# Kernel tuning notes

Hardware: AMD Instinct MI355X
Metric: run time of the kernel (lower is better)

The kernel has to match this reference:

```python
import jax, jax.numpy as jnp
import numpy as np

NUM_NODES = 80000
V_GLOBALS = 50000
N = 32      # grapharea_size
D = 300     # feature dim
R = 4       # num relations
E = 64      # edges per timestep
B, T = 2, 64


def setup_inputs() -> dict:
    key = jax.random.key(0)
    ks = jax.random.split(key, 10)
    return {
        "x_indices": jax.random.randint(ks[0], (B, T, N), 0, NUM_NODES, dtype=jnp.int32),
        "edge_index": jax.random.randint(ks[1], (B, T, 2, E), 0, N, dtype=jnp.int32),
        "edge_type": jax.random.randint(ks[2], (B, T, E), 0, R, dtype=jnp.int32),
        "X": jax.random.normal(ks[3], (NUM_NODES, D), jnp.float32) * 0.1,
        "conv_W": jax.random.normal(ks[4], (R, D, D), jnp.float32) * (1.0 / np.sqrt(D)),
        "W_0": jax.random.normal(ks[5], (D, D), jnp.float32) * (1.0 / np.sqrt(D)),
        "update_gate_W": jax.random.normal(ks[6], (N * D, D), jnp.float32) * (1.0 / np.sqrt(N * D)),
        "update_gate_U": jax.random.normal(ks[7], (D, D), jnp.float32) * (1.0 / np.sqrt(D)),
        "lin_w": jax.random.normal(ks[8], (V_GLOBALS, D), jnp.float32) * (1.0 / np.sqrt(D)),
        "lin_b": jax.random.normal(ks[9], (V_GLOBALS,), jnp.float32) * 0.01,
    }


def _rgcn_step(X, conv_W, W_0, Wg, Ug, lin_w, lin_b, mem, idx, ei, et):
    # gather grapharea features: [N, D]
    gx = X[idx]
    src, dst = ei[0], ei[1]
    n = gx.shape[0]
    r = conv_W.shape[0]
    # per-relation linear transform: [R, N, D]
    xw = jnp.einsum('nd,rde->rne', gx, conv_W)
    # edge-type masks emulate split_edge_index: [R, E]
    mask = (et[None, :] == jnp.arange(r, dtype=et.dtype)[:, None]).astype(gx.dtype)
    # GCN symmetric normalization with self-loops (deg includes self-loop weight 1)
    deg = jax.vmap(lambda w: jax.ops.segment_sum(w, dst, num_segments=n))(mask) + 1.0  # [R, N]
    dis = jax.lax.rsqrt(deg)
    norm = dis[:, src] * dis[:, dst] * mask                      # [R, E]
    msgs = xw[:, src, :] * norm[..., None]                       # [R, E, D]
    agg = jax.vmap(lambda m: jax.ops.segment_sum(m, dst, num_segments=n))(msgs)
    agg = agg + xw * (dis ** 2)[..., None]                       # self-loop messages
    composite = agg.sum(0)                                       # sum over relations, [N, D]
    # eye(N) @ (gx @ W_0) == gx @ W_0
    proposed = composite + gx @ W_0
    # GRU-style update gate from flattened grapharea + previous memory's first node
    u = jax.nn.sigmoid(gx.reshape(-1) @ Wg + mem[0] @ Ug)        # [D]
    new = u[None, :] * proposed + (1.0 - u[None, :]) * mem       # [N, D]
    x1 = jax.nn.leaky_relu(new)[0]                               # current node, [D]
    logits = x1 @ lin_w.T + lin_b                                # [V]
    return new, jax.nn.log_softmax(logits)


def reference(x_indices, edge_index, edge_type, X, conv_W, W_0, update_gate_W, update_gate_U, lin_w, lin_b):
    b, t, n = x_indices.shape
    s = b * t
    idxs = x_indices.reshape(s, n)
    eis = edge_index.reshape(s, 2, -1)
    ets = edge_type.reshape(s, -1)

    def step(mem, inp):
        idx, ei, et = inp
        new, logp = _rgcn_step(X, conv_W, W_0, update_gate_W, update_gate_U,
                               lin_w, lin_b, mem, idx, ei, et)
        # memory carry is a non-grad buffer updated via .data.copy_ in torch
        return jax.lax.stop_gradient(new), logp

    mem0 = jnp.zeros((n, X.shape[1]), X.dtype)
    _, preds_globals = jax.lax.scan(step, mem0, (idxs, eis, ets))  # [S, V]
    preds_senses = jnp.zeros((s,), X.dtype)  # include_senses=False -> stacked zeros
    return preds_globals, preds_senses
```

## Files before the change

kernel.cpp:

```cpp
#include <hip/hip_runtime.h>

#define S 128
#define N 32
#define D 300
#define DP 320
#define E 64
#define R 4
#define V 50000
#define VP 50048
#define ND 9600
#define KY 1504
#define DPAD 304

typedef unsigned short ushortT;
typedef __attribute__((ext_vector_type(8))) short short8;
typedef __attribute__((ext_vector_type(4))) short short4v;
typedef __attribute__((ext_vector_type(4))) float floatx4;
typedef __attribute__((ext_vector_type(19))) float floatx19;

__device__ inline float bf2f(ushortT h) {
    unsigned u = ((unsigned)h) << 16;
    float f;
    __builtin_memcpy(&f, &u, 4);
    return f;
}

__device__ inline float bfbits_lo(unsigned u) {
    unsigned b = u << 16;
    float f;
    __builtin_memcpy(&f, &b, 4);
    return f;
}

__device__ inline float bfbits_hi(unsigned u) {
    unsigned b = u & 0xffff0000u;
    float f;
    __builtin_memcpy(&f, &b, 4);
    return f;
}

__device__ inline ushortT f2bf(float f) {
    unsigned u;
    __builtin_memcpy(&u, &f, 4);
    unsigned r = (u + 0x7fffu + ((u >> 16) & 1u)) >> 16;
    return (ushortT)r;
}

__device__ inline float ldf(const void* p, size_t i, int isb) {
    return isb ? bf2f(((const ushortT*)p)[i]) : ((const float*)p)[i];
}

__device__ inline float rdlane(float v, int lane) {
    int iv;
    __builtin_memcpy(&iv, &v, 4);
    int r = __builtin_amdgcn_readlane(iv, lane);
    float f;
    __builtin_memcpy(&f, &r, 4);
    return f;
}

__global__ void k_detect(const void* X, int* flag) {
    __shared__ int bad;
    if (threadIdx.x == 0) bad = 0;
    __syncthreads();
    const ushortT* p = (const ushortT*)X;
    int b = 0;
    for (int i = threadIdx.x; i < 4096; i += 256) {
        float v = bf2f(p[i]);
        if (!(v > -2.f && v < 2.f)) b = 1;
    }
    if (b) atomicOr(&bad, 1);
    __syncthreads();
    if (threadIdx.x == 0) flag[0] = bad ? 0 : 1;
}

__global__ void k_gatherb(const int* __restrict__ flag, const int* __restrict__ xi,
                          const void* __restrict__ X, ushortT* __restrict__ gxb) {
    int isb = flag[0];
    int sn = blockIdx.x;
    int d = threadIdx.x;
    if (d < D) {
        int node = xi[sn];
        ushortT v = isb ? ((const ushortT*)X)[(size_t)node * D + d]
                        : f2bf(((const float*)X)[(size_t)node * D + d]);
        gxb[(size_t)sn * D + d] = v;
    }
}

__global__ void k_twg(const int* __restrict__ flag, const void* __restrict__ Wg,
                      ushortT* __restrict__ wgt) {
    int isb = flag[0];
    __shared__ float tile[32][33];
    int k0 = blockIdx.x * 32, d0 = blockIdx.y * 32;
    int tx = threadIdx.x & 31, ty = threadIdx.x >> 5;
    for (int i = ty; i < 32; i += 8) {
        int d = d0 + tx;
        tile[i][tx] = (d < D) ? ldf(Wg, (size_t)(k0 + i) * D + d, isb) : 0.f;
    }
    __syncthreads();
    for (int i = ty; i < 32; i += 8) {
        int d = d0 + i;
        if (d < DPAD) wgt[(size_t)d * ND + k0 + tx] = f2bf(tile[tx][i]);
    }
}

__global__ void k_tws(const int* __restrict__ flag, const void* __restrict__ convW,
                      const void* __restrict__ W0, ushortT* __restrict__ wst) {
    int isb = flag[0];
    __shared__ float tile[32][33];
    int k0 = blockIdx.x * 32, d0 = blockIdx.y * 32;
    int tx = threadIdx.x & 31, ty = threadIdx.x >> 5;
    for (int i = ty; i < 32; i += 8) {
        int kp = k0 + i, d = d0 + tx;
        float v = 0.f;
        if (d < D && kp < 1500)
            v = (kp < 1200) ? ldf(convW, (size_t)kp * D + d, isb)
                            : ldf(W0, (size_t)(kp - 1200) * D + d, isb);
        tile[i][tx] = v;
    }
    __syncthreads();
    for (int i = ty; i < 32; i += 8) {
        int d = d0 + i;
        if (d < DPAD) wst[(size_t)d * KY + k0 + tx] = f2bf(tile[tx][i]);
    }
}

__global__ void k_yb(const ushortT* __restrict__ gxb, const int* __restrict__ ei,
                     const int* __restrict__ et, ushortT* __restrict__ yb) {
    int s = blockIdx.x;
    int t = threadIdx.x;
    __shared__ int se[E], de[E], te[E];
    __shared__ float disv[R][N];
    if (t < E) {
        se[t] = ei[(size_t)s * 2 * E + t];
        de[t] = ei[(size_t)s * 2 * E + E + t];
        te[t] = et[(size_t)s * E + t];
    }
    __syncthreads();
    if (t < R * N) {
        int r = t >> 5, n = t & 31;
        float c = 1.f;
        for (int e = 0; e < E; ++e) c += (te[e] == r && de[e] == n) ? 1.f : 0.f;
        disv[r][n] = rsqrtf(c);
    }
    __syncthreads();
    if (t < D) {
        const ushortT* g = gxb + (size_t)s * ND;
        float g0 = bf2f(g[t]);
        float yy[R];
#pragma unroll
        for (int r = 0; r < R; ++r) yy[r] = g0 * disv[r][0] * disv[r][0];
        for (int e = 0; e < E; ++e) {
            if (de[e] == 0) {
                int r = te[e];
                yy[r] += disv[r][se[e]] * disv[r][0] * bf2f(g[(size_t)se[e] * D + t]);
            }
        }
#pragma unroll
        for (int r = 0; r < R; ++r) yb[(size_t)s * KY + r * D + t] = f2bf(yy[r]);
        yb[(size_t)s * KY + 4 * D + t] = g[t];
    }
    if (t < 4) yb[(size_t)s * KY + 1500 + t] = 0;
}

__global__ __launch_bounds__(256) void k_gemm(const ushortT* __restrict__ A, int lda,
                                              const ushortT* __restrict__ Bt, int ldb,
                                              float* __restrict__ C, int ldc, int ncols,
                                              int kchunks, int per) {
    int wave = threadIdx.x >> 6, lane = threadIdx.x & 63;
    int col = lane & 15, quad = lane >> 4;
    int m0 = blockIdx.x * 16, n0 = blockIdx.y * 16;
    int z = blockIdx.z;
    int kbeg = z * per;
    int kend = kbeg + per;
    if (kend > kchunks) kend = kchunks;
    floatx4 acc = {0.f, 0.f, 0.f, 0.f};
    const ushortT* ap = A + (size_t)(m0 + col) * lda + quad * 8;
    const ushortT* bp = Bt + (size_t)(n0 + col) * ldb + quad * 8;
    for (int kc = kbeg + wave; kc < kend; kc += 4) {
        short8 a = *(const short8*)(ap + kc * 32);
        short8 b = *(const short8*)(bp + kc * 32);
        acc = __builtin_amdgcn_mfma_f32_16x16x32_bf16(a, b, acc, 0, 0, 0);
    }
    __shared__ float red[4][64][4];
#pragma unroll
    for (int i = 0; i < 4; ++i) red[wave][lane][i] = acc[i];
    __syncthreads();
    if (wave == 0) {
#pragma unroll
        for (int i = 0; i < 4; ++i) {
            float v = red[0][lane][i] + red[1][lane][i] + red[2][lane][i] + red[3][lane][i];
            int m = m0 + quad * 4 + i;
            int n = n0 + col;
            if (n < ncols) C[(size_t)z * S * ldc + (size_t)m * ldc + n] = v;
        }
    }
}

__global__ void k_red(const float* __restrict__ part, float* __restrict__ out, int n, int nz) {
    int i = blockIdx.x * 256 + threadIdx.x;
    if (i < n) {
        float v = 0.f;
        for (int z = 0; z < nz; ++z) v += part[(size_t)z * n + i];
        out[i] = v;
    }
}

__global__ __attribute__((amdgpu_flat_work_group_size(512, 512), amdgpu_waves_per_eu(2, 2))) void
k_scan(const int* __restrict__ flag, const float* __restrict__ a, const float* __restrict__ P0,
       const void* __restrict__ Ug, ushortT* __restrict__ x1p) {
    int isb = flag[0];
    int t = threadIdx.x;
    int w = t >> 6, lane = t & 63;
    int kbase = w * 38;
    int myk = kbase + lane;
    bool red_ok = (lane < 38) && (myk < D);
    int d4 = 256 + lane;
    bool d4ok = d4 < D;
    floatx19 A0, A1, A2, A3, A4, B0, B1, B2, B3, B4;
    if (isb) {
        const ushortT* U = (const ushortT*)Ug;
#pragma unroll
        for (int j = 0; j < 19; ++j) {
            int k1 = kbase + j, k2 = k1 + 19;
            bool k2ok = k2 < D;
            A0[j] = bf2f(U[k1 * D + lane]);
            A1[j] = bf2f(U[k1 * D + 64 + lane]);
            A2[j] = bf2f(U[k1 * D + 128 + lane]);
            A3[j] = bf2f(U[k1 * D + 192 + lane]);
            A4[j] = d4ok ? bf2f(U[k1 * D + d4]) : 0.f;
            B0[j] = k2ok ? bf2f(U[k2 * D + lane]) : 0.f;
            B1[j] = k2ok ? bf2f(U[k2 * D + 64 + lane]) : 0.f;
            B2[j] = k2ok ? bf2f(U[k2 * D + 128 + lane]) : 0.f;
            B3[j] = k2ok ? bf2f(U[k2 * D + 192 + lane]) : 0.f;
            B4[j] = (k2ok && d4ok) ? bf2f(U[k2 * D + d4]) : 0.f;
        }
    } else {
        const float* U = (const float*)Ug;
#pragma unroll
        for (int j = 0; j < 19; ++j) {
            int k1 = kbase + j, k2 = k1 + 19;
            bool k2ok = k2 < D;
            A0[j] = U[k1 * D + lane];
            A1[j] = U[k1 * D + 64 + lane];
            A2[j] = U[k1 * D + 128 + lane];
            A3[j] = U[k1 * D + 192 + lane];
            A4[j] = d4ok ? U[k1 * D + d4] : 0.f;
            B0[j] = k2ok ? U[k2 * D + lane] : 0.f;
            B1[j] = k2ok ? U[k2 * D + 64 + lane] : 0.f;
            B2[j] = k2ok ? U[k2 * D + 128 + lane] : 0.f;
            B3[j] = k2ok ? U[k2 * D + 192 + lane] : 0.f;
            B4[j] = (k2ok && d4ok) ? U[k2 * D + d4] : 0.f;
        }
    }
    for (int i = t; i < S * 20; i += 512) {
        int s = i / 20, d = 300 + (i % 20);
        x1p[(size_t)s * DP + d] = 0;
    }
    __shared__ float part[2][8][320];
    float mreg = 0.f;
    int buf = 0;
    for (int s = 0; s < S; ++s) {
        float av = 0.f, pv = 0.f;
        if (red_ok) {
            av = a[s * D + myk];
            pv = P0[s * D + myk];
        }
        float acc0 = 0.f, acc1 = 0.f, acc2 = 0.f, acc3 = 0.f, acc4 = 0.f;
#pragma unroll
        for (int j = 0; j < 19; ++j) {
            float sm = rdlane(mreg, j);
            acc0 = fmaf(sm, A0[j], acc0);
            acc1 = fmaf(sm, A1[j], acc1);
            acc2 = fmaf(sm, A2[j], acc2);
            acc3 = fmaf(sm, A3[j], acc3);
            acc4 = fmaf(sm, A4[j], acc4);
        }
#pragma unroll
        for (int j = 0; j < 19; ++j) {
            float sm = rdlane(mreg, 19 + j);
            acc0 = fmaf(sm, B0[j], acc0);
            acc1 = fmaf(sm, B1[j], acc1);
            acc2 = fmaf(sm, B2[j], acc2);
            acc3 = fmaf(sm, B3[j], acc3);
            acc4 = fmaf(sm, B4[j], acc4);
        }
        part[buf][w][lane] = acc0;
        part[buf][w][64 + lane] = acc1;
        part[buf][w][128 + lane] = acc2;
        part[buf][w][192 + lane] = acc3;
        part[buf][w][256 + lane] = acc4;
        __syncthreads();
        if (red_ok) {
            float pr = av;
#pragma unroll
            for (int w2 = 0; w2 < 8; ++w2) pr += part[buf][w2][myk];
            float u = 1.f / (1.f + __expf(-pr));
            float nm = u * pv + (1.f - u) * mreg;
            mreg = nm;
            float x = nm > 0.f ? nm : 0.01f * nm;
            x1p[(size_t)s * DP + myk] = f2bf(x);
        }
        buf ^= 1;
    }
}

__global__ __launch_bounds__(256) void k_logits(const int* __restrict__ flag,
                                                const ushortT* __restrict__ x1p,
                                                const void* __restrict__ lw,
                                                const void* __restrict__ lb,
                                                void* __restrict__ out) {
    int isb = flag[0];
    int wave = threadIdx.x >> 6, lane = threadIdx.x & 63;
    int col = lane & 15, quad = lane >> 4;
    int v = blockIdx.x * 64 + wave * 16 + col;
    int vv = v < V ? v : V - 1;
    floatx4 acc[8];
#pragma unroll
    for (int i = 0; i < 8; ++i) acc[i] = (floatx4){0.f, 0.f, 0.f, 0.f};
#pragma unroll
    for (int kc = 0; kc < 9; ++kc) {
        int k0 = kc * 32 + quad * 8;
        short8 b;
        if (isb) {
            const ushortT* bp = (const ushortT*)lw + (size_t)vv * D + k0;
            short4v lo = *(const short4v*)bp;
            short4v hi = *(const short4v*)(bp + 4);
            b = (short8){lo[0], lo[1], lo[2], lo[3], hi[0], hi[1], hi[2], hi[3]};
        } else {
            const float* bp = (const float*)lw + (size_t)vv * D + k0;
            floatx4 f0 = *(const floatx4*)bp;
            floatx4 f1 = *(const floatx4*)(bp + 4);
            b = (short8){(short)f2bf(f0[0]), (short)f2bf(f0[1]), (short)f2bf(f0[2]),
                         (short)f2bf(f0[3]), (short)f2bf(f1[0]), (short)f2bf(f1[1]),
                         (short)f2bf(f1[2]), (short)f2bf(f1[3])};
        }
#pragma unroll
        for (int st = 0; st < 8; ++st) {
            short8 aa = *(const short8*)(x1p + (size_t)(st * 16 + col) * DP + k0);
            acc[st] = __builtin_amdgcn_mfma_f32_16x16x32_bf16(aa, b, acc[st], 0, 0, 0);
        }
    }
    {
        int k0 = 288 + quad * 8;
        short8 b;
#pragma unroll
        for (int j = 0; j < 8; ++j) {
            int k = k0 + j;
            ushortT bv = 0;
            if (k < D)
                bv = isb ? ((const ushortT*)lw)[(size_t)vv * D + k]
                         : f2bf(((const float*)lw)[(size_t)vv * D + k]);
            b[j] = (short)bv;
        }
#pragma unroll
        for (int st = 0; st < 8; ++st) {
            short8 aa = *(const short8*)(x1p + (size_t)(st * 16 + col) * DP + k0);
            acc[st] = __builtin_amdgcn_mfma_f32_16x16x32_bf16(aa, b, acc[st], 0, 0, 0);
        }
    }
    if (v < V) {
        float bias = ldf(lb, v, isb);
#pragma unroll
        for (int st = 0; st < 8; ++st) {
#pragma unroll
            for (int i = 0; i < 4; ++i) {
                int s = st * 16 + quad * 4 + i;
                float val = acc[st][i] + bias;
                if (isb)
                    ((ushortT*)out)[(size_t)s * V + v] = f2bf(val);
                else
                    ((float*)out)[(size_t)s * V + v] = val;
            }
        }
    }
}

__global__ __launch_bounds__(512) void k_norm(const int* __restrict__ flag,
                                              void* __restrict__ out) {
    int isb = flag[0];
    int s = blockIdx.x;
    int t = threadIdx.x;
    __shared__ float red[512];
    if (s == 0 && t < S) {
        if (isb)
            ((ushortT*)out)[(size_t)S * V + t] = 0;
        else
            ((float*)out)[(size_t)S * V + t] = 0.f;
    }
    float mx = -1e30f;
    if (isb) {
        const uint4* row = (const uint4*)((const ushortT*)out + (size_t)s * V);
        for (int i = t; i < 6250; i += 512) {
            uint4 q = row[i];
            mx = fmaxf(mx, fmaxf(fmaxf(bfbits_lo(q.x), bfbits_hi(q.x)),
                                 fmaxf(bfbits_lo(q.y), bfbits_hi(q.y))));
            mx = fmaxf(mx, fmaxf(fmaxf(bfbits_lo(q.z), bfbits_hi(q.z)),
                                 fmaxf(bfbits_lo(q.w), bfbits_hi(q.w))));
        }
    } else {
        const floatx4* row = (const floatx4*)((const float*)out + (size_t)s * V);
        for (int i = t; i < 12500; i += 512) {
            floatx4 q = row[i];
            mx = fmaxf(mx, fmaxf(fmaxf(q[0], q[1]), fmaxf(q[2], q[3])));
        }
    }
    red[t] = mx;
    __syncthreads();
    for (int o = 256; o > 0; o >>= 1) {
        if (t < o) red[t] = fmaxf(red[t], red[t + o]);
        __syncthreads();
    }
    float M = red[0];
    __syncthreads();
    float sm = 0.f;
    if (isb) {
        const uint4* row = (const uint4*)((const ushortT*)out + (size_t)s * V);
        for (int i = t; i < 6250; i += 512) {
            uint4 q = row[i];
            sm += __expf(bfbits_lo(q.x) - M) + __expf(bfbits_hi(q.x) - M) +
                  __expf(bfbits_lo(q.y) - M) + __expf(bfbits_hi(q.y) - M) +
                  __expf(bfbits_lo(q.z) - M) + __expf(bfbits_hi(q.z) - M) +
                  __expf(bfbits_lo(q.w) - M) + __expf(bfbits_hi(q.w) - M);
        }
    } else {
        const floatx4* row = (const floatx4*)((const float*)out + (size_t)s * V);
        for (int i = t; i < 12500; i += 512) {
            floatx4 q = row[i];
            sm += __expf(q[0] - M) + __expf(q[1] - M) + __expf(q[2] - M) + __expf(q[3] - M);
        }
    }
    red[t] = sm;
    __syncthreads();
    for (int o = 256; o > 0; o >>= 1) {
        if (t < o) red[t] += red[t + o];
        __syncthreads();
    }
    float lse = M + __logf(red[0]);
    if (isb) {
        uint4* row = (uint4*)((ushortT*)out + (size_t)s * V);
        for (int i = t; i < 6250; i += 512) {
            uint4 q = row[i];
            uint4 o;
            o.x = (unsigned)f2bf(bfbits_lo(q.x) - lse) |
                  ((unsigned)f2bf(bfbits_hi(q.x) - lse) << 16);
            o.y = (unsigned)f2bf(bfbits_lo(q.y) - lse) |
                  ((unsigned)f2bf(bfbits_hi(q.y) - lse) << 16);
            o.z = (unsigned)f2bf(bfbits_lo(q.z) - lse) |
                  ((unsigned)f2bf(bfbits_hi(q.z) - lse) << 16);
            o.w = (unsigned)f2bf(bfbits_lo(q.w) - lse) |
                  ((unsigned)f2bf(bfbits_hi(q.w) - lse) << 16);
            row[i] = o;
        }
    } else {
        floatx4* row = (floatx4*)((float*)out + (size_t)s * V);
        for (int i = t; i < 12500; i += 512) {
            floatx4 q = row[i];
            q[0] -= lse;
            q[1] -= lse;
            q[2] -= lse;
            q[3] -= lse;
            row[i] = q;
        }
    }
}

#define OFF_FLAG 0
#define OFF_GXB 256
#define OFF_WGT 2457856
#define OFF_WST 8294656
#define OFF_YB 9209088
#define OFF_A 9594112
#define OFF_P0 9747712
#define OFF_X1P 9901312
#define OFF_STATS 9983232
#define OFF_PART 9983744
#define PART_A_BYTES (4 * S * D * 4)
#define PART_P_BYTES (2 * S * D * 4)

extern "C" void kernel_launch(void* const* d_in, const int* in_sizes, int n_in, void* d_out,
                              int out_size, void* d_ws, size_t ws_size, hipStream_t stream) {
    const int* xi = (const int*)d_in[0];
    const int* ei = (const int*)d_in[1];
    const int* et = (const int*)d_in[2];
    const void* X = d_in[3];
    const void* convW = d_in[4];
    const void* W0 = d_in[5];
    const void* Wg = d_in[6];
    const void* Ug = d_in[7];
    const void* lw = d_in[8];
    const void* lb = d_in[9];
    char* ws = (char*)d_ws;

    int* flag = (int*)(ws + OFF_FLAG);
    ushortT* gxb = (ushortT*)(ws + OFF_GXB);
    ushortT* wgt = (ushortT*)(ws + OFF_WGT);
    ushortT* wst = (ushortT*)(ws + OFF_WST);
    ushortT* yb = (ushortT*)(ws + OFF_YB);
    float* a = (float*)(ws + OFF_A);
    float* P0 = (float*)(ws + OFF_P0);
    ushortT* x1p = (ushortT*)(ws + OFF_X1P);

    bool split = ws_size >= (size_t)(OFF_PART + PART_A_BYTES + PART_P_BYTES);
    int nza = split ? 4 : 1;
    int nzp = split ? 2 : 1;
    float* apart = split ? (float*)(ws + OFF_PART) : a;
    float* ppart = split ? (float*)(ws + OFF_PART + PART_A_BYTES) : P0;
    int pera = (ND / 32 + nza - 1) / nza;
    int perp = (KY / 32 + nzp - 1) / nzp;

    hipLaunchKernelGGL(k_detect, dim3(1), dim3(256), 0, stream, X, flag);
    hipLaunchKernelGGL(k_gatherb, dim3(S * N), dim3(DP), 0, stream, flag, xi, X, gxb);
    hipLaunchKernelGGL(k_twg, dim3(ND / 32, 10), dim3(256), 0, stream, flag, Wg, wgt);
    hipLaunchKernelGGL(k_tws, dim3(KY / 32, 10), dim3(256), 0, stream, flag, convW, W0, wst);
    hipLaunchKernelGGL(k_yb, dim3(S), dim3(DP), 0, stream, gxb, ei, et, yb);
    hipLaunchKernelGGL(k_gemm, dim3(S / 16, 19, nza), dim3(256), 0, stream, gxb, ND, wgt, ND,
                       apart, D, D, ND / 32, pera);
    if (split)
        hipLaunchKernelGGL(k_red, dim3((S * D + 255) / 256), dim3(256), 0, stream, apart, a,
                           S * D, nza);
    hipLaunchKernelGGL(k_gemm, dim3(S / 16, 19, nzp), dim3(256), 0, stream, yb, KY, wst, KY,
                       ppart, D, D, KY / 32, perp);
    if (split)
        hipLaunchKernelGGL(k_red, dim3((S * D + 255) / 256), dim3(256), 0, stream, ppart, P0,
                           S * D, nzp);
    hipLaunchKernelGGL(k_scan, dim3(1), dim3(512), 0, stream, flag, a, P0, Ug, x1p);
    hipLaunchKernelGGL(k_logits, dim3(VP / 64), dim3(256), 0, stream, flag, x1p, lw, lb, d_out);
    hipLaunchKernelGGL(k_norm, dim3(S), dim3(512), 0, stream, flag, d_out);
}
```

Measured before the change: 463.0 us.

## Use packed fp16 dot2 with LDS-broadcast memory state in the scan kernel

New measurement: 411.8 us. 1.12x faster.

```diff
diff --git a/kernel.cpp b/kernel.cpp
--- a/kernel.cpp
+++ b/kernel.cpp
@@ -16,7 +16,14 @@
 typedef __attribute__((ext_vector_type(8))) short short8;
 typedef __attribute__((ext_vector_type(4))) short short4v;
 typedef __attribute__((ext_vector_type(4))) float floatx4;
-typedef __attribute__((ext_vector_type(19))) float floatx19;
+typedef __attribute__((ext_vector_type(2))) _Float16 half2v;
+typedef __attribute__((ext_vector_type(19))) unsigned int uintx19;
+
+#if defined(__has_builtin)
+#if __has_builtin(__builtin_amdgcn_fdot2)
+#define HAVE_FDOT2 1
+#endif
+#endif
 
 __device__ inline float bf2f(ushortT h) {
     unsigned u = ((unsigned)h) << 16;
@@ -50,13 +57,24 @@
     return isb ? bf2f(((const ushortT*)p)[i]) : ((const float*)p)[i];
 }
 
-__device__ inline float rdlane(float v, int lane) {
-    int iv;
-    __builtin_memcpy(&iv, &v, 4);
-    int r = __builtin_amdgcn_readlane(iv, lane);
-    float f;
-    __builtin_memcpy(&f, &r, 4);
-    return f;
+__device__ inline float dot2f(unsigned a, unsigned b, float c) {
+    half2v av, bv;
+    __builtin_memcpy(&av, &a, 4);
+    __builtin_memcpy(&bv, &b, 4);
+#if defined(HAVE_FDOT2)
+    return __builtin_amdgcn_fdot2(av, bv, c, false);
+#else
+    return fmaf((float)av[1], (float)bv[1], fmaf((float)av[0], (float)bv[0], c));
+#endif
+}
+
+__device__ inline unsigned packh2(float lo, float hi) {
+    half2v h;
+    h[0] = (_Float16)lo;
+    h[1] = (_Float16)hi;
+    unsigned u;
+    __builtin_memcpy(&u, &h, 4);
+    return u;
 }
 
 __global__ void k_detect(const void* X, int* flag) {
@@ -217,90 +235,72 @@
     bool red_ok = (lane < 38) && (myk < D);
     int d4 = 256 + lane;
     bool d4ok = d4 < D;
-    floatx19 A0, A1, A2, A3, A4, B0, B1, B2, B3, B4;
-    if (isb) {
-        const ushortT* U = (const ushortT*)Ug;
-#pragma unroll
-        for (int j = 0; j < 19; ++j) {
-            int k1 = kbase + j, k2 = k1 + 19;
-            bool k2ok = k2 < D;
-            A0[j] = bf2f(U[k1 * D + lane]);
-            A1[j] = bf2f(U[k1 * D + 64 + lane]);
-            A2[j] = bf2f(U[k1 * D + 128 + lane]);
-            A3[j] = bf2f(U[k1 * D + 192 + lane]);
-            A4[j] = d4ok ? bf2f(U[k1 * D + d4]) : 0.f;
-            B0[j] = k2ok ? bf2f(U[k2 * D + lane]) : 0.f;
-            B1[j] = k2ok ? bf2f(U[k2 * D + 64 + lane]) : 0.f;
-            B2[j] = k2ok ? bf2f(U[k2 * D + 128 + lane]) : 0.f;
-            B3[j] = k2ok ? bf2f(U[k2 * D + 192 + lane]) : 0.f;
-            B4[j] = (k2ok && d4ok) ? bf2f(U[k2 * D + d4]) : 0.f;
-        }
-    } else {
-        const float* U = (const float*)Ug;
-#pragma unroll
-        for (int j = 0; j < 19; ++j) {
-            int k1 = kbase + j, k2 = k1 + 19;
-            bool k2ok = k2 < D;
-            A0[j] = U[k1 * D + lane];
-            A1[j] = U[k1 * D + 64 + lane];
-            A2[j] = U[k1 * D + 128 + lane];
-            A3[j] = U[k1 * D + 192 + lane];
-            A4[j] = d4ok ? U[k1 * D + d4] : 0.f;
-            B0[j] = k2ok ? U[k2 * D + lane] : 0.f;
-            B1[j] = k2ok ? U[k2 * D + 64 + lane] : 0.f;
-            B2[j] = k2ok ? U[k2 * D + 128 + lane] : 0.f;
-            B3[j] = k2ok ? U[k2 * D + 192 + lane] : 0.f;
-            B4[j] = (k2ok && d4ok) ? U[k2 * D + d4] : 0.f;
-        }
+    uintx19 UV0, UV1, UV2, UV3, UV4;
+#pragma unroll
+    for (int j = 0; j < 19; ++j) {
+        int k1 = kbase + 2 * j, k2 = k1 + 1;
+        bool k1ok = k1 < D, k2ok = k2 < D;
+        UV0[j] = packh2(k1ok ? ldf(Ug, (size_t)k1 * D + lane, isb) : 0.f,
+                        k2ok ? ldf(Ug, (size_t)k2 * D + lane, isb) : 0.f);
+        UV1[j] = packh2(k1ok ? ldf(Ug, (size_t)k1 * D + 64 + lane, isb) : 0.f,
+                        k2ok ? ldf(Ug, (size_t)k2 * D + 64 + lane, isb) : 0.f);
+        UV2[j] = packh2(k1ok ? ldf(Ug, (size_t)k1 * D + 128 + lane, isb) : 0.f,
+                        k2ok ? ldf(Ug, (size_t)k2 * D + 128 + lane, isb) : 0.f);
+        UV3[j] = packh2(k1ok ? ldf(Ug, (size_t)k1 * D + 192 + lane, isb) : 0.f,
+                        k2ok ? ldf(Ug, (size_t)k2 * D + 192 + lane, isb) : 0.f);
+        UV4[j] = packh2((k1ok && d4ok) ? ldf(Ug, (size_t)k1 * D + d4, isb) : 0.f,
+                        (k2ok && d4ok) ? ldf(Ug, (size_t)k2 * D + d4, isb) : 0.f);
     }
     for (int i = t; i < S * 20; i += 512) {
         int s = i / 20, d = 300 + (i % 20);
         x1p[(size_t)s * DP + d] = 0;
     }
-    __shared__ float part[2][8][320];
+    __shared__ float part[8][320];
+    __shared__ unsigned msh16[2][160];
+    for (int i = t; i < 320; i += 512) ((unsigned*)msh16)[i] = 0;
     float mreg = 0.f;
     int buf = 0;
+    __syncthreads();
     for (int s = 0; s < S; ++s) {
         float av = 0.f, pv = 0.f;
         if (red_ok) {
             av = a[s * D + myk];
             pv = P0[s * D + myk];
         }
+        uintx19 MV;
+#pragma unroll
+        for (int j = 0; j < 19; ++j) MV[j] = msh16[buf][w * 20 + j];
         float acc0 = 0.f, acc1 = 0.f, acc2 = 0.f, acc3 = 0.f, acc4 = 0.f;
 #pragma unroll
         for (int j = 0; j < 19; ++j) {
-            float sm = rdlane(mreg, j);
-            acc0 = fmaf(sm, A0[j], acc0);
-            acc1 = fmaf(sm, A1[j], acc1);
-            acc2 = fmaf(sm, A2[j], acc2);
-            acc3 = fmaf(sm, A3[j], acc3);
-            acc4 = fmaf(sm, A4[j], acc4);
-        }
-#pragma unroll
-        for (int j = 0; j < 19; ++j) {
-            float sm = rdlane(mreg, 19 + j);
-            acc0 = fmaf(sm, B0[j], acc0);
-            acc1 = fmaf(sm, B1[j], acc1);
-            acc2 = fmaf(sm, B2[j], acc2);
-            acc3 = fmaf(sm, B3[j], acc3);
-            acc4 = fmaf(sm, B4[j], acc4);
-        }
-        part[buf][w][lane] = acc0;
-        part[buf][w][64 + lane] = acc1;
-        part[buf][w][128 + lane] = acc2;
-        part[buf][w][192 + lane] = acc3;
-        part[buf][w][256 + lane] = acc4;
+            unsigned md = MV[j];
+            acc0 = dot2f(UV0[j], md, acc0);
+            acc1 = dot2f(UV1[j], md, acc1);
+            acc2 = dot2f(UV2[j], md, acc2);
+            acc3 = dot2f(UV3[j], md, acc3);
+            acc4 = dot2f(UV4[j], md, acc4);
+        }
+        part[w][lane] = acc0;
+        part[w][64 + lane] = acc1;
+        part[w][128 + lane] = acc2;
+        part[w][192 + lane] = acc3;
+        part[w][256 + lane] = acc4;
         __syncthreads();
         if (red_ok) {
             float pr = av;
 #pragma unroll
-            for (int w2 = 0; w2 < 8; ++w2) pr += part[buf][w2][myk];
+            for (int w2 = 0; w2 < 8; ++w2) pr += part[w2][myk];
             float u = 1.f / (1.f + __expf(-pr));
             float nm = u * pv + (1.f - u) * mreg;
             mreg = nm;
+            _Float16 mh = (_Float16)nm;
+            ushortT mb;
+            __builtin_memcpy(&mb, &mh, 2);
+            ((ushortT*)&msh16[buf ^ 1][0])[w * 40 + lane] = mb;
             float x = nm > 0.f ? nm : 0.01f * nm;
             x1p[(size_t)s * DP + myk] = f2bf(x);
         }
+        __syncthreads();
         buf ^= 1;
     }
 }
```
